# Optimization experiments

Measured on AMD Instinct MI355X. Metric: run time of the kernel, lower is better.

Reference implementation:

```python
import jax, jax.numpy as jnp
import numpy as np

B, SQ, SK, D_MODEL, H, D = 2, 2048, 2048, 1024, 16, 64


def setup_inputs() -> dict:
    key = jax.random.key(0)
    ks = jax.random.split(key, 10)
    s = 1.0 / np.sqrt(D_MODEL)
    return {
        "x": jax.random.normal(ks[0], (B, SK, D_MODEL), jnp.float32),
        "x2": jax.random.normal(ks[1], (B, SQ, D_MODEL), jnp.float32),
        "Wq": jax.random.normal(ks[2], (H, D_MODEL, D), jnp.float32) * s,
        "bq": jax.random.normal(ks[3], (H, D), jnp.float32) * s,
        "Wk": jax.random.normal(ks[4], (H, D_MODEL, D), jnp.float32) * s,
        "bk": jax.random.normal(ks[5], (H, D), jnp.float32) * s,
        "Wv": jax.random.normal(ks[6], (H, D_MODEL, D), jnp.float32) * s,
        "bv": jax.random.normal(ks[7], (H, D), jnp.float32) * s,
        "Wo": jax.random.normal(ks[8], (D_MODEL, D_MODEL), jnp.float32) * s,
        "bo": jax.random.normal(ks[9], (D_MODEL,), jnp.float32) * s,
    }


def reference(x, x2, Wq, bq, Wk, bk, Wv, bv, Wo, bo):
    # Batched per-head projections (fuses the Python per-head loop).
    # q: [B, H, SQ, D]; k,v: [B, H, SK, D]
    q = jnp.einsum("bsm,hmd->bhsd", x2, Wq) + bq[None, :, None, :]
    k = jnp.einsum("bsm,hmd->bhsd", x, Wk) + bk[None, :, None, :]
    v = jnp.einsum("bsm,hmd->bhsd", x, Wv) + bv[None, :, None, :]
    scale = 1.0 / jnp.sqrt(jnp.asarray(D, q.dtype))
    scores = jnp.einsum("bhqd,bhkd->bhqk", q, k) * scale  # [B,H,SQ,SK]
    attn = jax.nn.softmax(scores, axis=-1)
    o = jnp.einsum("bhqk,bhkd->bhqd", attn, v)  # [B,H,SQ,D]
    # concat heads along feature dim (head-major order matches torch.cat)
    o = o.transpose(0, 2, 1, 3).reshape(B, SQ, H * D)
    # final projection; dropout is identity in eval mode
    return o @ Wo.T + bo
```

## Files before the change

kernel.cpp:

```cpp
#include <hip/hip_runtime.h>
#include <math.h>

#define B_   2
#define SQ_  2048
#define SK_  2048
#define DM_  1024
#define H_   16
#define D_   64

typedef __attribute__((ext_vector_type(8))) short bf16x8;
typedef __attribute__((ext_vector_type(4))) float f32x4;
typedef unsigned int u32;

__device__ __forceinline__ short f2bf(float f) {
    union { float f; unsigned u; } v; v.f = f;
    unsigned r = v.u + 0x7FFFu + ((v.u >> 16) & 1u);
    return (short)(r >> 16);
}
__device__ __forceinline__ u32 pk2bf(float x, float y) {
    union { float f; u32 u; } a, b; a.f = x; b.f = y;
    return ((a.u + 0x8000u) >> 16) | ((b.u + 0x8000u) & 0xFFFF0000u);
}
__device__ __forceinline__ u32 pkbf_rh(float x, float y) {
    union { float f; u32 u; } a, b; a.f = x; b.f = y;
    return __builtin_amdgcn_perm(b.u + 0x8000u, a.u + 0x8000u, 0x07060302u);
}

__device__ __forceinline__ void gll16(const void* g, void* l) {
    __builtin_amdgcn_global_load_lds(
        (const __attribute__((address_space(1))) u32*)g,
        (__attribute__((address_space(3))) u32*)l, 16, 0, 0);
}

__global__ __launch_bounds__(256) void prep_kernel(
    const float* __restrict__ Wq, const float* __restrict__ Wk,
    const float* __restrict__ Wv, const float* __restrict__ Wo,
    const float* __restrict__ x,  const float* __restrict__ x2,
    short* __restrict__ WqT, short* __restrict__ WkT,
    short* __restrict__ WvT, short* __restrict__ Wob,
    short* __restrict__ xb,  short* __restrict__ x2b)
{
    const int t = threadIdx.x;
    const int z = blockIdx.z;
    if (z >= 3) {
        const float* src = (z == 3) ? Wo : (z == 4) ? x : x2;
        short* dst       = (z == 3) ? Wob : (z == 4) ? xb : x2b;
        int nloop = (z == 3) ? 4 : 16;
        int bid = blockIdx.y * 16 + blockIdx.x;
        #pragma unroll 4
        for (int j = 0; j < nloop; j++) {
            int i = bid * (nloop * 256) + j * 256 + t;
            float4 v = ((const float4*)src)[i];
            short4 s;
            s.x = f2bf(v.x); s.y = f2bf(v.y); s.z = f2bf(v.z); s.w = f2bf(v.w);
            ((short4*)dst)[i] = s;
        }
        return;
    }
    const float* W = (z == 0) ? Wq : (z == 1) ? Wk : Wv;
    short* WT      = (z == 0) ? WqT : (z == 1) ? WkT : WvT;
    const int h  = blockIdx.y;
    const int m0 = blockIdx.x * 64;
    __shared__ short Ls[64][68];

    #pragma unroll
    for (int it = 0; it < 4; it++) {
        int lin = it * 256 + t;
        int m = lin >> 4, d4 = lin & 15;
        float4 v = *(const float4*)&W[((long)h * DM_ + m0 + m) * D_ + d4 * 4];
        short4 s;
        s.x = f2bf(v.x); s.y = f2bf(v.y); s.z = f2bf(v.z); s.w = f2bf(v.w);
        *(short4*)&Ls[m][d4 * 4] = s;
    }
    __syncthreads();
    #pragma unroll
    for (int it = 0; it < 2; it++) {
        int d = (t >> 3) + it * 32, scol = t & 7;
        bf16x8 vv;
        #pragma unroll
        for (int j = 0; j < 8; j++) vv[j] = Ls[scol * 8 + j][d];
        *(bf16x8*)&WT[((long)h * 64 + d) * DM_ + m0 + scol * 8] = vv;
    }
}

__device__ __forceinline__ void gemm_stage(
    short* __restrict__ Asb, short* __restrict__ Bsb,
    const short* __restrict__ A, const short* __restrict__ Bw,
    int r0, int n0, int k0c, int w, int srow, int sc)
{
    #pragma unroll
    for (int j = 0; j < 4; j++) {
        int q   = w * 4 + j;
        int row = q * 8 + srow;
        gll16(A  + ((long)(r0 + row) << 10) + k0c + sc * 8, Asb + q * 512);
        gll16(Bw + ((long)(n0 + row) << 10) + k0c + sc * 8, Bsb + q * 512);
    }
}

template <int MODE>
__device__ __forceinline__ void gemm_core(
    short* __restrict__ Ls,
    const short* __restrict__ A, const short* __restrict__ Bw,
    const float* __restrict__ bias, void* __restrict__ outp,
    int r0, int n0, float oscale)
{
    const int t    = threadIdx.x;
    const int w    = t >> 6;
    const int ln   = t & 63;
    const int l15  = ln & 15;
    const int quad = ln >> 4;
    const int wr   = w >> 1;
    const int wc   = w & 1;

    f32x4 acc[4][4];
    #pragma unroll
    for (int i = 0; i < 4; i++)
        #pragma unroll
        for (int j = 0; j < 4; j++) acc[i][j] = (f32x4){0.f, 0.f, 0.f, 0.f};

    const int srow = ln >> 3;
    const int sc   = (ln & 7) ^ srow;
    const int rsw  = l15 & 7;

    gemm_stage(Ls, Ls + 8192, A, Bw, r0, n0, 0, w, srow, sc);

    int cur = 0;
    for (int k0 = 0; k0 < 1024; k0 += 64) {
        __syncthreads();
        if (k0 + 64 < 1024) {
            short* Anx = Ls + (cur ^ 1) * 16384;
            gemm_stage(Anx, Anx + 8192, A, Bw, r0, n0, k0 + 64, w, srow, sc);
        }
        const short* Asb = Ls + cur * 16384;
        const short* Bsb = Asb + 8192;
        #pragma unroll
        for (int kh = 0; kh < 2; kh++) {
            bf16x8 af[4], bfr[4];
            #pragma unroll
            for (int i = 0; i < 4; i++) {
                int ra = wr * 64 + i * 16 + l15;
                int rb = wc * 64 + i * 16 + l15;
                int pc = ((kh * 4 + quad) ^ rsw) * 8;
                af[i]  = *(const bf16x8*)&Asb[ra * 64 + pc];
                bfr[i] = *(const bf16x8*)&Bsb[rb * 64 + pc];
            }
            #pragma unroll
            for (int i = 0; i < 4; i++)
                #pragma unroll
                for (int j = 0; j < 4; j++)
                    acc[i][j] = __builtin_amdgcn_mfma_f32_16x16x32_bf16(
                        af[i], bfr[j], acc[i][j], 0, 0, 0);
        }
        cur ^= 1;
    }

    #pragma unroll
    for (int j = 0; j < 4; j++) {
        int col = n0 + wc * 64 + j * 16 + l15;
        float bv = bias[col];
        if (MODE == 2) {
            int hh = col >> 6, dd = col & 63;
            #pragma unroll
            for (int i = 0; i < 4; i++) {
                int rowb = r0 + wr * 64 + i * 16 + quad * 4;
                int bb = rowb >> 11, ss = rowb & 2047;
                int sl = ss & 63;
                int sp = (ss & ~63) | (sl & 35) | ((sl & 12) << 1) | ((sl & 16) >> 2);
                short4 sv;
                sv.x = f2bf(acc[i][j][0] + bv);
                sv.y = f2bf(acc[i][j][1] + bv);
                sv.z = f2bf(acc[i][j][2] + bv);
                sv.w = f2bf(acc[i][j][3] + bv);
                *(short4*)&((short*)outp)[
                    ((long)(((bb << 4) + hh) * 64 + dd) << 11) + sp] = sv;
            }
        } else {
            #pragma unroll
            for (int i = 0; i < 4; i++) {
                int rowb = r0 + wr * 64 + i * 16 + quad * 4;
                #pragma unroll
                for (int r = 0; r < 4; r++) {
                    float v = (acc[i][j][r] + bv) * oscale;
                    if (MODE == 0)
                        ((short*)outp)[(long)(rowb + r) * 1024 + col] = f2bf(v);
                    else
                        ((float*)outp)[(long)(rowb + r) * 1024 + col] = v;
                }
            }
        }
    }
}

#define QSCALE 0.180336880977f

__global__ __launch_bounds__(256) void gemm_qkv_kernel(
    const short* __restrict__ x2b, const short* __restrict__ xb,
    const short* __restrict__ WqT, const short* __restrict__ WkT,
    const short* __restrict__ WvT,
    const float* __restrict__ bq, const float* __restrict__ bk,
    const float* __restrict__ bv,
    short* __restrict__ Qb, short* __restrict__ Kb, short* __restrict__ VT)
{
    __shared__ short Ls[2 * 16384];
    const int z = blockIdx.z;
    if (z == 0) {
        gemm_core<0>(Ls, x2b, WqT, bq, Qb, blockIdx.x * 128, blockIdx.y * 128, QSCALE);
    } else if (z == 1) {
        gemm_core<0>(Ls, xb, WkT, bk, Kb, blockIdx.x * 128, blockIdx.y * 128, 1.0f);
    } else {
        gemm_core<2>(Ls, xb, WvT, bv, VT, blockIdx.x * 128, blockIdx.y * 128, 1.0f);
    }
}

__device__ __forceinline__ void gout_stage(
    short* __restrict__ Asb, short* __restrict__ Bsb,
    const short* __restrict__ A, const short* __restrict__ Bw,
    int r0, int n0, int k0c, int w, int srow, int sc)
{
    #pragma unroll
    for (int j = 0; j < 6; j++) {
        int q = w * 6 + j;
        if (q < 8) {
            int row = q * 8 + srow;
            gll16(A + ((long)(r0 + row) << 10) + k0c + sc * 8, Asb + q * 512);
        } else {
            int qb = q - 8;
            int row = qb * 8 + srow;
            gll16(Bw + ((long)(n0 + row) << 10) + k0c + sc * 8, Bsb + qb * 512);
        }
    }
}

__global__ __launch_bounds__(256) void gemm_out_kernel(
    const short* __restrict__ A, const short* __restrict__ Bw,
    const float* __restrict__ bias, float* __restrict__ outp)
{
    __shared__ short Ls[2 * 12288];

    const int r0   = blockIdx.x * 64;
    const int n0   = blockIdx.y * 128;
    const int t    = threadIdx.x;
    const int w    = t >> 6;
    const int ln   = t & 63;
    const int l15  = ln & 15;
    const int quad = ln >> 4;
    const int wr   = w >> 1;
    const int wc   = w & 1;

    f32x4 acc[2][4];
    #pragma unroll
    for (int i = 0; i < 2; i++)
        #pragma unroll
        for (int j = 0; j < 4; j++) acc[i][j] = (f32x4){0.f, 0.f, 0.f, 0.f};

    const int srow = ln >> 3;
    const int sc   = (ln & 7) ^ srow;
    const int rsw  = l15 & 7;

    gout_stage(Ls, Ls + 4096, A, Bw, r0, n0, 0, w, srow, sc);

    int cur = 0;
    for (int k0 = 0; k0 < 1024; k0 += 64) {
        __syncthreads();
        if (k0 + 64 < 1024) {
            short* Anx = Ls + (cur ^ 1) * 12288;
            gout_stage(Anx, Anx + 4096, A, Bw, r0, n0, k0 + 64, w, srow, sc);
        }
        const short* Asb = Ls + cur * 12288;
        const short* Bsb = Asb + 4096;
        #pragma unroll
        for (int kh = 0; kh < 2; kh++) {
            int pc = ((kh * 4 + quad) ^ rsw) * 8;
            bf16x8 af[2], bfr[4];
            #pragma unroll
            for (int i = 0; i < 2; i++)
                af[i] = *(const bf16x8*)&Asb[(wr * 32 + i * 16 + l15) * 64 + pc];
            #pragma unroll
            for (int j = 0; j < 4; j++)
                bfr[j] = *(const bf16x8*)&Bsb[(wc * 64 + j * 16 + l15) * 64 + pc];
            #pragma unroll
            for (int i = 0; i < 2; i++)
                #pragma unroll
                for (int j = 0; j < 4; j++)
                    acc[i][j] = __builtin_amdgcn_mfma_f32_16x16x32_bf16(
                        af[i], bfr[j], acc[i][j], 0, 0, 0);
        }
        cur ^= 1;
    }

    #pragma unroll
    for (int j = 0; j < 4; j++) {
        int col = n0 + wc * 64 + j * 16 + l15;
        float bv = bias[col];
        #pragma unroll
        for (int i = 0; i < 2; i++) {
            int rowb = r0 + wr * 32 + i * 16 + quad * 4;
            #pragma unroll
            for (int r = 0; r < 4; r++)
                outp[(long)(rowb + r) * 1024 + col] = acc[i][j][r] + bv;
        }
    }
}

__global__ __launch_bounds__(256, 2) void flash_kernel(
    const short* __restrict__ Q, const short* __restrict__ K,
    const short* __restrict__ VT, short* __restrict__ O)
{
    const int t    = threadIdx.x;
    const int wave = t >> 6;
    const int ln   = t & 63;
    const int l15  = ln & 15;
    const int quad = ln >> 4;
    const int bh = blockIdx.y;
    const int b  = bh >> 4;
    const int h  = bh & 15;
    const int q0 = blockIdx.x * 128;
    const int wq = q0 + wave * 32;

    __shared__ short Ks[2][2][64 * 64];
    __shared__ short Vs[2][2][64 * 64];

    const int srow = ln >> 3;
    const int sc   = (ln & 7) ^ srow;
    const int rsw  = l15 & 7;
    const int pc0  = ((quad    ) ^ rsw) * 8;
    const int pc1  = ((quad + 4) ^ rsw) * 8;
    const int rb   = l15 * 64;

    bf16x8 aQ0[2], aQ1[2];
    #pragma unroll
    for (int qg = 0; qg < 2; qg++) {
        const short* Qp = Q + ((long)(b * SQ_ + wq + qg * 16 + l15)) * 1024
                            + h * 64 + quad * 8;
        aQ0[qg] = *(const bf16x8*)(Qp);
        aQ1[qg] = *(const bf16x8*)(Qp + 32);
    }

    bf16x8 ones;
    #pragma unroll
    for (int j = 0; j < 8; j++) ones[j] = (short)0x3F80;

    const f32x4 fz = (f32x4){0.f, 0.f, 0.f, 0.f};

    f32x4 o_acc[2][4];
    f32x4 l_acc[2];
    #pragma unroll
    for (int qg = 0; qg < 2; qg++) {
        l_acc[qg] = fz;
        #pragma unroll
        for (int i = 0; i < 4; i++) o_acc[qg][i] = fz;
    }

    const short* Kbase = K  + ((long)b * SK_) * 1024 + h * 64;
    const short* Vbase = VT + (long)bh * D_ * SK_;
    const int qqa = wave * 2, qqb = wave * 2 + 1;
    const int rowa = qqa * 8 + srow, rowb_ = qqb * 8 + srow;

    #define STAGE(bufp, half, kbase)                                            \
        gll16(Kbase + (long)((kbase) + rowa)  * 1024 + sc * 8,                  \
              &Ks[bufp][half][qqa * 512]);                                      \
        gll16(Kbase + (long)((kbase) + rowb_) * 1024 + sc * 8,                  \
              &Ks[bufp][half][qqb * 512]);                                      \
        gll16(Vbase + (long)rowa  * 2048 + (kbase) + sc * 8,                    \
              &Vs[bufp][half][qqa * 512]);                                      \
        gll16(Vbase + (long)rowb_ * 2048 + (kbase) + sc * 8,                    \
              &Vs[bufp][half][qqb * 512]);

    STAGE(0, 0, 0)
    STAGE(0, 1, 64)

    int cur = 0;
    for (int k0 = 0; k0 < SK_; k0 += 128) {
        __syncthreads();
        if (k0 + 128 < SK_) {
            int nx = cur ^ 1;
            STAGE(nx, 0, k0 + 128)
            STAGE(nx, 1, k0 + 192)
        }
        const short* K0 = &Ks[cur][0][0];
        const short* K1 = &Ks[cur][1][0];
        const short* V0 = &Vs[cur][0][0];
        const short* V1 = &Vs[cur][1][0];

        bf16x8 kfA[8];
        #pragma unroll
        for (int kt = 0; kt < 4; kt++) {
            const short* kr = &K0[kt * 1024 + rb];
            kfA[kt * 2    ] = *(const bf16x8*)&kr[pc0];
            kfA[kt * 2 + 1] = *(const bf16x8*)&kr[pc1];
        }

        bf16x8 kfB[8];
        #pragma unroll
        for (int kt = 0; kt < 4; kt++) {
            const short* kr = &K1[kt * 1024 + rb];
            kfB[kt * 2    ] = *(const bf16x8*)&kr[pc0];
            kfB[kt * 2 + 1] = *(const bf16x8*)&kr[pc1];
        }
        f32x4 zA[2][4], zB[2][4];
        #pragma unroll
        for (int kt = 0; kt < 4; kt++)
            #pragma unroll
            for (int qg = 0; qg < 2; qg++) {
                f32x4 z = __builtin_amdgcn_mfma_f32_16x16x32_bf16(kfA[kt * 2], aQ0[qg], fz, 0, 0, 0);
                zA[qg][kt] = __builtin_amdgcn_mfma_f32_16x16x32_bf16(kfA[kt * 2 + 1], aQ1[qg], z, 0, 0, 0);
            }

        bf16x8 vfA[8];
        #pragma unroll
        for (int dt = 0; dt < 4; dt++) {
            const short* vr = &V0[dt * 1024 + rb];
            vfA[dt * 2    ] = *(const bf16x8*)&vr[pc0];
            vfA[dt * 2 + 1] = *(const bf16x8*)&vr[pc1];
        }
        u32 pwA[2][8], pwB[2][8];
        #pragma unroll
        for (int kt = 0; kt < 4; kt++) {
            #pragma unroll
            for (int qg = 0; qg < 2; qg++) {
                f32x4 z = __builtin_amdgcn_mfma_f32_16x16x32_bf16(kfB[kt * 2], aQ0[qg], fz, 0, 0, 0);
                zB[qg][kt] = __builtin_amdgcn_mfma_f32_16x16x32_bf16(kfB[kt * 2 + 1], aQ1[qg], z, 0, 0, 0);
            }
            #pragma unroll
            for (int qg = 0; qg < 2; qg++) {
                f32x4 s = zA[qg][kt];
                pwA[qg][kt * 2    ] = pkbf_rh(__builtin_amdgcn_exp2f(s[0]),
                                              __builtin_amdgcn_exp2f(s[1]));
                pwA[qg][kt * 2 + 1] = pkbf_rh(__builtin_amdgcn_exp2f(s[2]),
                                              __builtin_amdgcn_exp2f(s[3]));
            }
        }

        bf16x8 aP0A[2], aP1A[2];
        #pragma unroll
        for (int qg = 0; qg < 2; qg++) {
            union { bf16x8 v; u32 w[4]; } u0, u1;
            u0.w[0] = pwA[qg][0]; u0.w[1] = pwA[qg][1];
            u0.w[2] = pwA[qg][2]; u0.w[3] = pwA[qg][3];
            u1.w[0] = pwA[qg][4]; u1.w[1] = pwA[qg][5];
            u1.w[2] = pwA[qg][6]; u1.w[3] = pwA[qg][7];
            aP0A[qg] = u0.v; aP1A[qg] = u1.v;
            l_acc[qg] = __builtin_amdgcn_mfma_f32_16x16x32_bf16(aP0A[qg], ones, l_acc[qg], 0, 0, 0);
            l_acc[qg] = __builtin_amdgcn_mfma_f32_16x16x32_bf16(aP1A[qg], ones, l_acc[qg], 0, 0, 0);
        }

        bf16x8 vfB[8];
        #pragma unroll
        for (int dt = 0; dt < 4; dt++) {
            const short* vr = &V1[dt * 1024 + rb];
            vfB[dt * 2    ] = *(const bf16x8*)&vr[pc0];
            vfB[dt * 2 + 1] = *(const bf16x8*)&vr[pc1];
        }
        #pragma unroll
        for (int dt = 0; dt < 4; dt++) {
            #pragma unroll
            for (int qg = 0; qg < 2; qg++) {
                o_acc[qg][dt] = __builtin_amdgcn_mfma_f32_16x16x32_bf16(aP0A[qg], vfA[dt * 2    ], o_acc[qg][dt], 0, 0, 0);
                o_acc[qg][dt] = __builtin_amdgcn_mfma_f32_16x16x32_bf16(aP1A[qg], vfA[dt * 2 + 1], o_acc[qg][dt], 0, 0, 0);
            }
            #pragma unroll
            for (int qg = 0; qg < 2; qg++) {
                f32x4 s = zB[qg][dt];
                pwB[qg][dt * 2    ] = pkbf_rh(__builtin_amdgcn_exp2f(s[0]),
                                              __builtin_amdgcn_exp2f(s[1]));
                pwB[qg][dt * 2 + 1] = pkbf_rh(__builtin_amdgcn_exp2f(s[2]),
                                              __builtin_amdgcn_exp2f(s[3]));
            }
        }

        bf16x8 aP0B[2], aP1B[2];
        #pragma unroll
        for (int qg = 0; qg < 2; qg++) {
            union { bf16x8 v; u32 w[4]; } u0, u1;
            u0.w[0] = pwB[qg][0]; u0.w[1] = pwB[qg][1];
            u0.w[2] = pwB[qg][2]; u0.w[3] = pwB[qg][3];
            u1.w[0] = pwB[qg][4]; u1.w[1] = pwB[qg][5];
            u1.w[2] = pwB[qg][6]; u1.w[3] = pwB[qg][7];
            aP0B[qg] = u0.v; aP1B[qg] = u1.v;
        }
        __builtin_amdgcn_s_setprio(1);
        #pragma unroll
        for (int qg = 0; qg < 2; qg++) {
            l_acc[qg] = __builtin_amdgcn_mfma_f32_16x16x32_bf16(aP0B[qg], ones, l_acc[qg], 0, 0, 0);
            l_acc[qg] = __builtin_amdgcn_mfma_f32_16x16x32_bf16(aP1B[qg], ones, l_acc[qg], 0, 0, 0);
        }
        #pragma unroll
        for (int dt = 0; dt < 4; dt++) {
            #pragma unroll
            for (int qg = 0; qg < 2; qg++) {
                o_acc[qg][dt] = __builtin_amdgcn_mfma_f32_16x16x32_bf16(aP0B[qg], vfB[dt * 2    ], o_acc[qg][dt], 0, 0, 0);
                o_acc[qg][dt] = __builtin_amdgcn_mfma_f32_16x16x32_bf16(aP1B[qg], vfB[dt * 2 + 1], o_acc[qg][dt], 0, 0, 0);
            }
        }
        __builtin_amdgcn_s_setprio(0);
        cur ^= 1;
    }
    #undef STAGE

    #pragma unroll
    for (int qg = 0; qg < 2; qg++) {
        #pragma unroll
        for (int r = 0; r < 4; r++) {
            float inv = 1.0f / l_acc[qg][r];
            long row = (long)b * SQ_ + wq + qg * 16 + quad * 4 + r;
            short* Op = O + row * 1024 + h * 64 + l15;
            #pragma unroll
            for (int dt = 0; dt < 4; dt++)
                Op[dt * 16] = f2bf(o_acc[qg][dt][r] * inv);
        }
    }
}

extern "C" void kernel_launch(void* const* d_in, const int* in_sizes, int n_in,
                              void* d_out, int out_size, void* d_ws, size_t ws_size,
                              hipStream_t stream) {
    const float* x  = (const float*)d_in[0];
    const float* x2 = (const float*)d_in[1];
    const float* Wq = (const float*)d_in[2];
    const float* bq = (const float*)d_in[3];
    const float* Wk = (const float*)d_in[4];
    const float* bk = (const float*)d_in[5];
    const float* Wv = (const float*)d_in[6];
    const float* bv = (const float*)d_in[7];
    const float* Wo = (const float*)d_in[8];
    const float* bo = (const float*)d_in[9];
    float* out = (float*)d_out;

    const size_t nAct = (size_t)B_ * SK_ * DM_;
    const size_t nW   = (size_t)DM_ * DM_;
    short* bufA = (short*)d_ws;
    short* bufB = bufA + nAct;
    short* Qb   = bufB + nAct;
    short* Kb   = Qb + nAct;
    short* VTws = Kb + nAct;
    short* WqT  = VTws + nAct;
    short* WkT  = WqT + nW;
    short* WvT  = WkT + nW;
    short* Wob  = WvT + nW;

    prep_kernel<<<dim3(16, 16, 6), 256, 0, stream>>>(
        Wq, Wk, Wv, Wo, x, x2, WqT, WkT, WvT, Wob, bufA, bufB);

    gemm_qkv_kernel<<<dim3(32, 8, 3), 256, 0, stream>>>(
        bufB, bufA, WqT, WkT, WvT, bq, bk, bv, Qb, Kb, VTws);

    flash_kernel<<<dim3(16, 32), 256, 0, stream>>>(Qb, Kb, VTws, bufB);
    gemm_out_kernel<<<dim3(64, 8), 256, 0, stream>>>(bufB, Wob, bo, out);
}
```

Before: 198.2 us.

## Swizzle block indices for XCD locality and defer second-half PV MFMAs

Both the QKV GEMM and the flash kernel remap the linear block id so that blocks landing on the same XCD (round-robin dispatch) handle neighbouring tiles or the same batch-head, improving L2 reuse of K/V and weights. The flash loop is also software-pipelined. The P·V and row-sum MFMAs for the second 64-key half are carried in registers (pwB, vfB) and issued at the start of the next iteration, with an epilogue after the loop. This overlaps those MFMAs with the next tile's QK and exp work, at the cost of more live registers, which could cause spills at launch bounds (256,2).

```diff
diff --git a/kernel.cpp b/kernel.cpp
--- a/kernel.cpp
+++ b/kernel.cpp
@@ -202,13 +202,17 @@
     short* __restrict__ Qb, short* __restrict__ Kb, short* __restrict__ VT)
 {
     __shared__ short Ls[2 * 16384];
+    const int f  = blockIdx.x + (blockIdx.y << 5);
+    const int wi = ((f & 7) << 5) | (f >> 3);
+    const int bx = wi & 31;
+    const int by = wi >> 5;
     const int z = blockIdx.z;
     if (z == 0) {
-        gemm_core<0>(Ls, x2b, WqT, bq, Qb, blockIdx.x * 128, blockIdx.y * 128, QSCALE);
+        gemm_core<0>(Ls, x2b, WqT, bq, Qb, bx * 128, by * 128, QSCALE);
     } else if (z == 1) {
-        gemm_core<0>(Ls, xb, WkT, bk, Kb, blockIdx.x * 128, blockIdx.y * 128, 1.0f);
+        gemm_core<0>(Ls, xb, WkT, bk, Kb, bx * 128, by * 128, 1.0f);
     } else {
-        gemm_core<2>(Ls, xb, WvT, bv, VT, blockIdx.x * 128, blockIdx.y * 128, 1.0f);
+        gemm_core<2>(Ls, xb, WvT, bv, VT, bx * 128, by * 128, 1.0f);
     }
 }
 
@@ -311,11 +315,13 @@
     const int ln   = t & 63;
     const int l15  = ln & 15;
     const int quad = ln >> 4;
-    const int bh = blockIdx.y;
-    const int b  = bh >> 4;
-    const int h  = bh & 15;
-    const int q0 = blockIdx.x * 128;
-    const int wq = q0 + wave * 32;
+    const int f   = blockIdx.x + (blockIdx.y << 4);
+    const int wid = ((f & 7) << 6) | (f >> 3);
+    const int bh  = wid >> 4;
+    const int b   = bh >> 4;
+    const int h   = bh & 15;
+    const int q0  = (wid & 15) * 128;
+    const int wq  = q0 + wave * 32;
 
     __shared__ short Ks[2][2][64 * 64];
     __shared__ short Vs[2][2][64 * 64];
@@ -369,6 +375,9 @@
     STAGE(0, 0, 0)
     STAGE(0, 1, 64)
 
+    u32 pwB[2][8];
+    bf16x8 vfB[8];
+
     int cur = 0;
     for (int k0 = 0; k0 < SK_; k0 += 128) {
         __syncthreads();
@@ -390,6 +399,34 @@
             kfA[kt * 2 + 1] = *(const bf16x8*)&kr[pc1];
         }
 
+        if (k0) {
+            bf16x8 aP0B[2], aP1B[2];
+            #pragma unroll
+            for (int qg = 0; qg < 2; qg++) {
+                union { bf16x8 v; u32 w[4]; } u0, u1;
+                u0.w[0] = pwB[qg][0]; u0.w[1] = pwB[qg][1];
+                u0.w[2] = pwB[qg][2]; u0.w[3] = pwB[qg][3];
+                u1.w[0] = pwB[qg][4]; u1.w[1] = pwB[qg][5];
+                u1.w[2] = pwB[qg][6]; u1.w[3] = pwB[qg][7];
+                aP0B[qg] = u0.v; aP1B[qg] = u1.v;
+            }
+            __builtin_amdgcn_s_setprio(1);
+            #pragma unroll
+            for (int qg = 0; qg < 2; qg++) {
+                l_acc[qg] = __builtin_amdgcn_mfma_f32_16x16x32_bf16(aP0B[qg], ones, l_acc[qg], 0, 0, 0);
+                l_acc[qg] = __builtin_amdgcn_mfma_f32_16x16x32_bf16(aP1B[qg], ones, l_acc[qg], 0, 0, 0);
+            }
+            #pragma unroll
+            for (int dt = 0; dt < 4; dt++) {
+                #pragma unroll
+                for (int qg = 0; qg < 2; qg++) {
+                    o_acc[qg][dt] = __builtin_amdgcn_mfma_f32_16x16x32_bf16(aP0B[qg], vfB[dt * 2    ], o_acc[qg][dt], 0, 0, 0);
+                    o_acc[qg][dt] = __builtin_amdgcn_mfma_f32_16x16x32_bf16(aP1B[qg], vfB[dt * 2 + 1], o_acc[qg][dt], 0, 0, 0);
+                }
+            }
+            __builtin_amdgcn_s_setprio(0);
+        }
+
         bf16x8 kfB[8];
         #pragma unroll
         for (int kt = 0; kt < 4; kt++) {
@@ -413,7 +450,7 @@
             vfA[dt * 2    ] = *(const bf16x8*)&vr[pc0];
             vfA[dt * 2 + 1] = *(const bf16x8*)&vr[pc1];
         }
-        u32 pwA[2][8], pwB[2][8];
+        u32 pwA[2][8];
         #pragma unroll
         for (int kt = 0; kt < 4; kt++) {
             #pragma unroll
@@ -444,7 +481,6 @@
             l_acc[qg] = __builtin_amdgcn_mfma_f32_16x16x32_bf16(aP1A[qg], ones, l_acc[qg], 0, 0, 0);
         }
 
-        bf16x8 vfB[8];
         #pragma unroll
         for (int dt = 0; dt < 4; dt++) {
             const short* vr = &V1[dt * 1024 + rb];
@@ -467,7 +503,11 @@
                                               __builtin_amdgcn_exp2f(s[3]));
             }
         }
-
+        cur ^= 1;
+    }
+    #undef STAGE
+
+    {
         bf16x8 aP0B[2], aP1B[2];
         #pragma unroll
         for (int qg = 0; qg < 2; qg++) {
@@ -477,10 +517,6 @@
             u1.w[0] = pwB[qg][4]; u1.w[1] = pwB[qg][5];
             u1.w[2] = pwB[qg][6]; u1.w[3] = pwB[qg][7];
             aP0B[qg] = u0.v; aP1B[qg] = u1.v;
-        }
-        __builtin_amdgcn_s_setprio(1);
-        #pragma unroll
-        for (int qg = 0; qg < 2; qg++) {
             l_acc[qg] = __builtin_amdgcn_mfma_f32_16x16x32_bf16(aP0B[qg], ones, l_acc[qg], 0, 0, 0);
             l_acc[qg] = __builtin_amdgcn_mfma_f32_16x16x32_bf16(aP1B[qg], ones, l_acc[qg], 0, 0, 0);
         }
@@ -492,10 +528,7 @@
                 o_acc[qg][dt] = __builtin_amdgcn_mfma_f32_16x16x32_bf16(aP1B[qg], vfB[dt * 2 + 1], o_acc[qg][dt], 0, 0, 0);
             }
         }
-        __builtin_amdgcn_s_setprio(0);
-        cur ^= 1;
-    }
-    #undef STAGE
+    }
 
     #pragma unroll
     for (int qg = 0; qg < 2; qg++) {
```

After: 200.9 us. About the same (+1.4%).
